# Kernel tuning notes

Measured on AMD Instinct MI355X. Metric: run time of the kernel, lower is better.

Reference implementation:

```python
import jax, jax.numpy as jnp
from jax import lax
import numpy as np

NUM_CLASS = 80
N_PROP = 256
C_FEAT, H_FEAT, W_FEAT = 1024, 50, 80
IMG_H, IMG_W = 800, 1280
POOL = 14
SPATIAL_SCALE = 0.0625
SCORE_THR = 0.5
NMS_THR = 0.7
K_PRE = 1000   # pre-NMS candidate cap (jit-static stand-in for boolean filter)
K_OUT = 200    # keep[:200] in source
BW = (10.0, 10.0, 5.0, 5.0)
SCALE_CLAMP = float(np.log(1000.0 / 16.0))


def setup_inputs() -> dict:
    key = jax.random.key(0)
    ks = jax.random.split(key, 9)
    features = jax.random.normal(ks[0], (1, C_FEAT, H_FEAT, W_FEAT), jnp.float32)
    x1 = jax.random.uniform(ks[1], (N_PROP,), minval=0.0, maxval=IMG_W - 64.0)
    y1 = jax.random.uniform(ks[2], (N_PROP,), minval=0.0, maxval=IMG_H - 64.0)
    w = jax.random.uniform(ks[3], (N_PROP,), minval=32.0, maxval=320.0)
    h = jax.random.uniform(ks[4], (N_PROP,), minval=32.0, maxval=320.0)
    proposals = jnp.stack([x1, y1, jnp.minimum(x1 + w, float(IMG_W)),
                           jnp.minimum(y1 + h, float(IMG_H))], axis=1)
    d_in = C_FEAT * POOL * POOL
    w_fc = jax.random.normal(ks[5], (d_in, 1024), jnp.float32) / np.sqrt(d_in)
    b_fc = jnp.zeros((1024,), jnp.float32)
    # scale class head up so softmax produces confident (>0.5) detections
    w_cls = jax.random.normal(ks[6], (1024, NUM_CLASS + 1), jnp.float32) * (8.0 / np.sqrt(1024))
    b_cls = jnp.zeros((NUM_CLASS + 1,), jnp.float32)
    w_box = jax.random.normal(ks[7], (1024, NUM_CLASS * 4), jnp.float32) / np.sqrt(1024)
    b_box = jnp.zeros((NUM_CLASS * 4,), jnp.float32)
    return {"features": features, "proposals": proposals, "w_fc": w_fc, "b_fc": b_fc,
            "w_cls": w_cls, "b_cls": b_cls, "w_box": w_box, "b_box": b_box}


def roi_align(features, rois):
    """torchvision RoIAlign (aligned=False), output 14x14, one sample per bin.
    features: [1,C,H,W], rois: [N,4] xyxy. Returns [N,C,14,14]."""
    f = features[0]                               # [C,H,W]
    H, W = f.shape[1], f.shape[2]
    x1 = rois[:, 0] * SPATIAL_SCALE
    y1 = rois[:, 1] * SPATIAL_SCALE
    x2 = rois[:, 2] * SPATIAL_SCALE
    y2 = rois[:, 3] * SPATIAL_SCALE
    rw = jnp.maximum(x2 - x1, 1.0)
    rh = jnp.maximum(y2 - y1, 1.0)
    bw = rw / POOL
    bh = rh / POOL
    grid = jnp.arange(POOL, dtype=jnp.float32) + 0.5
    xs = x1[:, None] + grid[None, :] * bw[:, None]      # [N,P] bin-center x
    ys = y1[:, None] + grid[None, :] * bh[:, None]      # [N,P] bin-center y
    Y = jnp.broadcast_to(ys[:, :, None], (rois.shape[0], POOL, POOL))
    X = jnp.broadcast_to(xs[:, None, :], (rois.shape[0], POOL, POOL))
    valid = (Y >= -1.0) & (Y <= H) & (X >= -1.0) & (X <= W)
    y = jnp.clip(Y, 0.0, H - 1.0)
    x = jnp.clip(X, 0.0, W - 1.0)
    y0 = jnp.floor(y).astype(jnp.int32)
    x0 = jnp.floor(x).astype(jnp.int32)
    y1i = jnp.minimum(y0 + 1, H - 1)
    x1i = jnp.minimum(x0 + 1, W - 1)
    ly = y - y0; lx = x - x0; hy = 1.0 - ly; hx = 1.0 - lx
    g = lambda yi, xi: f[:, yi, xi]               # -> [C,N,P,P]
    val = ((hy * hx) * g(y0, x0) + (hy * lx) * g(y0, x1i)
           + (ly * hx) * g(y1i, x0) + (ly * lx) * g(y1i, x1i))
    val = val * valid.astype(val.dtype)
    return jnp.transpose(val, (1, 0, 2, 3))       # [N,C,P,P]


def apply_deltas(boxes, deltas):
    """boxes,deltas: [..., 4]; detectron-style delta apply with weights BW."""
    w = boxes[..., 2] - boxes[..., 0]
    h = boxes[..., 3] - boxes[..., 1]
    cx = boxes[..., 0] + 0.5 * w
    cy = boxes[..., 1] + 0.5 * h
    dx = deltas[..., 0] / BW[0]
    dy = deltas[..., 1] / BW[1]
    dw = jnp.minimum(deltas[..., 2] / BW[2], SCALE_CLAMP)
    dh = jnp.minimum(deltas[..., 3] / BW[3], SCALE_CLAMP)
    pcx = dx * w + cx
    pcy = dy * h + cy
    pw = jnp.exp(dw) * w
    ph = jnp.exp(dh) * h
    return jnp.stack([pcx - 0.5 * pw, pcy - 0.5 * ph,
                      pcx + 0.5 * pw, pcy + 0.5 * ph], axis=-1)


def _iou_matrix(b):
    area = jnp.maximum(b[:, 2] - b[:, 0], 0.0) * jnp.maximum(b[:, 3] - b[:, 1], 0.0)
    lt = jnp.maximum(b[:, None, :2], b[None, :, :2])
    rb = jnp.minimum(b[:, None, 2:], b[None, :, 2:])
    wh = jnp.clip(rb - lt, 0.0)
    inter = wh[..., 0] * wh[..., 1]
    return inter / jnp.maximum(area[:, None] + area[None, :] - inter, 1e-9)


def forward(features, proposals, w_fc, b_fc, w_cls, b_cls, w_box, b_box):
    feat = roi_align(features, proposals)                 # [N,1024,14,14]
    x = feat.reshape(feat.shape[0], -1) @ w_fc + b_fc     # [N,1024]
    logits = x @ w_cls + b_cls                            # [N,81]
    deltas = x @ w_box + b_box                            # [N,320]
    scores = jax.nn.softmax(logits, axis=-1)[:, 1:]       # [N,80] drop bg

    # per-class box-delta apply (proposal expanded over classes)
    boxes = apply_deltas(jnp.broadcast_to(proposals[:, None, :], (N_PROP, NUM_CLASS, 4)),
                         deltas.reshape(N_PROP, NUM_CLASS, 4))
    boxes = jnp.stack([jnp.clip(boxes[..., 0], 0.0, float(IMG_W)),
                       jnp.clip(boxes[..., 1], 0.0, float(IMG_H)),
                       jnp.clip(boxes[..., 2], 0.0, float(IMG_W)),
                       jnp.clip(boxes[..., 3], 0.0, float(IMG_H))], axis=-1)

    # flatten (proposal, class) candidates; mask = score > 0.5 (boolean filter in source)
    s_flat = scores.reshape(-1)
    b_flat = boxes.reshape(-1, 4)
    c_flat = jnp.broadcast_to(jnp.arange(NUM_CLASS)[None, :], (N_PROP, NUM_CLASS)).reshape(-1)
    masked = jnp.where(s_flat > SCORE_THR, s_flat, -1.0)
    top_s, top_i = lax.top_k(masked, K_PRE)              # score-sorted candidates
    cand_b = b_flat[top_i]
    cand_c = c_flat[top_i]
    cand_valid = top_s > SCORE_THR

    # batched NMS: offset boxes by class so classes never interact
    off = cand_c.astype(jnp.float32) * float(IMG_W + 1)
    iou = _iou_matrix(cand_b + off[:, None])
    idxs = jnp.arange(K_PRE)

    def body(keep, xs):
        i, row = xs
        kept_i = keep[i]
        suppress = kept_i & (row > NMS_THR) & (idxs > i)
        return keep & ~suppress, kept_i

    _, kept = lax.scan(body, cand_valid, (idxs, iou))

    # compact kept candidates (already score-ordered) into top-200 slots
    rank = jnp.cumsum(kept.astype(jnp.int32)) - 1
    slot = jnp.where(kept, rank, K_OUT)  # out-of-range -> dropped
    out_boxes = jnp.zeros((K_OUT, 4), cand_b.dtype).at[slot].set(cand_b, mode='drop')
    out_scores = jnp.zeros((K_OUT,), top_s.dtype).at[slot].set(top_s, mode='drop')
    out_classes = jnp.full((K_OUT,), -1, jnp.int32).at[slot].set(cand_c.astype(jnp.int32), mode='drop')
    return out_boxes, out_scores, out_classes


def reference(features, proposals, w_fc, b_fc, w_cls, b_cls, w_box, b_box):
    return forward(features, proposals, w_fc, b_fc, w_cls, b_cls, w_box, b_box)
```

## Files before the change

kernel.cpp:

```cpp
#include <hip/hip_runtime.h>
#include <math.h>

#define N_PROP 256
#define NUM_CLASS 80
#define H_FEAT 50
#define W_FEAT 80
#define K_DIM 200704
#define D_HID 1024
#define SPATIAL_SCALE 0.0625f
#define SCALE_CLAMP 4.135166556742356f
#define IMG_W_F 1280.0f
#define IMG_H_F 800.0f

typedef unsigned short ushort_t;
typedef __attribute__((ext_vector_type(8))) short short8v;
typedef __attribute__((ext_vector_type(16))) float f32x16;
typedef __attribute__((ext_vector_type(4))) float f32x4v;
typedef __attribute__((ext_vector_type(4))) unsigned short ushort4v;
typedef __attribute__((ext_vector_type(2))) unsigned short ushort2v;

__device__ __forceinline__ unsigned short f2bf(float f) {
  unsigned int u = __builtin_bit_cast(unsigned int, f);
  u += 0x7FFFu + ((u >> 16) & 1u);
  return (unsigned short)(u >> 16);
}
__device__ __forceinline__ float bf2f(unsigned short h) {
  unsigned int u = ((unsigned int)h) << 16;
  return __builtin_bit_cast(float, u);
}

__global__ void roi_kernel(const float* __restrict__ F, const float* __restrict__ props,
                           ushort_t* __restrict__ Ahi, ushort_t* __restrict__ Alo) {
  const int tid = threadIdx.x;
  const int m = blockIdx.y;
  const int cg = blockIdx.x;
  __shared__ float w00[196], w01[196], w10[196], w11[196];
  __shared__ int o00[196], o01[196], o10[196], o11[196];
  const float x1s = props[m*4+0]*SPATIAL_SCALE;
  const float y1s = props[m*4+1]*SPATIAL_SCALE;
  const float x2s = props[m*4+2]*SPATIAL_SCALE;
  const float y2s = props[m*4+3]*SPATIAL_SCALE;
  const float bwf = fmaxf(x2s-x1s, 1.0f) / 14.0f;
  const float bhf = fmaxf(y2s-y1s, 1.0f) / 14.0f;
  if (tid < 196) {
    int ph = tid / 14, pw = tid - ph*14;
    float X = x1s + (pw + 0.5f)*bwf;
    float Y = y1s + (ph + 0.5f)*bhf;
    bool valid = (Y >= -1.0f) && (Y <= (float)H_FEAT) && (X >= -1.0f) && (X <= (float)W_FEAT);
    float x = fminf(fmaxf(X, 0.0f), (float)(W_FEAT-1));
    float y = fminf(fmaxf(Y, 0.0f), (float)(H_FEAT-1));
    float xf = floorf(x), yf = floorf(y);
    int ix0 = (int)xf, iy0 = (int)yf;
    int ix1 = min(ix0+1, W_FEAT-1), iy1 = min(iy0+1, H_FEAT-1);
    float lx = x-xf, ly = y-yf, hx = 1.0f-lx, hy = 1.0f-ly;
    float v = valid ? 1.0f : 0.0f;
    w00[tid] = hy*hx*v; w01[tid] = hy*lx*v; w10[tid] = ly*hx*v; w11[tid] = ly*lx*v;
    o00[tid] = iy0*W_FEAT+ix0; o01[tid] = iy0*W_FEAT+ix1;
    o10[tid] = iy1*W_FEAT+ix0; o11[tid] = iy1*W_FEAT+ix1;
  }
  __syncthreads();
  const int base_c = cg*128;
  const size_t rowbase = (size_t)m*K_DIM + (size_t)base_c*196;
  for (int it = 0; it < 49; ++it) {
    int i2 = it*512 + tid*2;
    int c = i2 / 196;
    int b = i2 - c*196;
    const float* f = F + (size_t)(base_c + c)*4000;
    float v0 = w00[b]*f[o00[b]] + w01[b]*f[o01[b]] + w10[b]*f[o10[b]] + w11[b]*f[o11[b]];
    float v1 = w00[b+1]*f[o00[b+1]] + w01[b+1]*f[o01[b+1]] + w10[b+1]*f[o10[b+1]] + w11[b+1]*f[o11[b+1]];
    unsigned short h0 = f2bf(v0), h1 = f2bf(v1);
    ushort2v hv; hv[0] = h0; hv[1] = h1;
    ushort2v lv; lv[0] = f2bf(v0 - bf2f(h0)); lv[1] = f2bf(v1 - bf2f(h1));
    *(ushort2v*)&Ahi[rowbase + i2] = hv;
    *(ushort2v*)&Alo[rowbase + i2] = lv;
  }
}

__global__ __launch_bounds__(512, 2) void mfma_gemm(
    const ushort_t* __restrict__ Ahi, const ushort_t* __restrict__ Alo,
    const float* __restrict__ B, float* __restrict__ P, int steps_per, int nwg) {
  __shared__ ushort_t lds[40960];
  const int tid = threadIdx.x;
  const int wv = tid >> 6, lane = tid & 63, l31 = lane & 31, lhi = lane >> 5;
  const int wm = wv >> 2, wn = wv & 3;
  int id = blockIdx.x;
  int nid = ((nwg & 7) == 0) ? ((id & 7) * (nwg >> 3) + (id >> 3)) : id;
  const int bn = (nid & 3) * 256;
  const int z  = nid >> 2;
  const int step0 = z * steps_per;
  int steps = steps_per;
  if (step0 + steps > 6272) steps = 6272 - step0;

  f32x16 acc[4][2];
  #pragma unroll
  for (int a = 0; a < 4; ++a)
    #pragma unroll
    for (int b = 0; b < 2; ++b)
      #pragma unroll
      for (int e = 0; e < 16; ++e) acc[a][b][e] = 0.0f;

  if (steps > 0) {
    const int H = steps * 2;
    const ushort_t* asrc[2];
    #pragma unroll
    for (int i = 0; i < 2; ++i) {
      int s = i*512 + tid;
      int plane = s >> 9, kb = (s >> 8) & 1, row = s & 255;
      const ushort_t* basep = plane ? Alo : Ahi;
      asrc[i] = basep + (size_t)row * K_DIM + step0*32 + kb*8;
    }
    const int p = tid >> 6, c4 = tid & 63;
    const bool bstage = (tid < 256);
    const float* bsrc = B + (size_t)(step0*32 + 4*p) * D_HID + bn + c4*4;
    const unsigned bkbh = (unsigned)(p >> 1) * 2048u, bsub = (unsigned)((p & 1) * 4);

    #define STAGE_A(aoff) do { \
      _Pragma("unroll") \
      for (int i = 0; i < 2; ++i) { \
        __builtin_amdgcn_global_load_lds(asrc[i], &lds[(aoff) + (unsigned)(i*512 + tid)*8u], 16, 0, 0); \
        asrc[i] += 16; } \
    } while (0)

    #define LOAD_B() do { \
      if (bstage) { \
        b0 = __builtin_nontemporal_load((const f32x4v*)(bsrc)); \
        b1 = __builtin_nontemporal_load((const f32x4v*)(bsrc + D_HID)); \
        b2 = __builtin_nontemporal_load((const f32x4v*)(bsrc + 2*D_HID)); \
        b3 = __builtin_nontemporal_load((const f32x4v*)(bsrc + 3*D_HID)); \
      } \
      bsrc += 16 * D_HID; \
    } while (0)

    #define WRITE_B(boff) do { \
      if (bstage) { \
        _Pragma("unroll") \
        for (int cc = 0; cc < 4; ++cc) { \
          float g0 = b0[cc], g1 = b1[cc], g2 = b2[cc], g3 = b3[cc]; \
          ushort4v hv, lv; \
          hv[0]=f2bf(g0); lv[0]=f2bf(g0-bf2f(hv[0])); \
          hv[1]=f2bf(g1); lv[1]=f2bf(g1-bf2f(hv[1])); \
          hv[2]=f2bf(g2); lv[2]=f2bf(g2-bf2f(hv[2])); \
          hv[3]=f2bf(g3); lv[3]=f2bf(g3-bf2f(hv[3])); \
          int col = c4*4 + cc, scol = col ^ ((col>>3)&7); \
          unsigned idx = (boff) + bkbh + (unsigned)scol*8u + bsub; \
          *(ushort4v*)&lds[idx] = hv; \
          *(ushort4v*)&lds[idx + 4096] = lv; \
        } \
      } \
    } while (0)

    #define COMPUTE(aoff, boff) do { \
      short8v ah[4], al[4], bh[2], bl[2]; \
      _Pragma("unroll") \
      for (int ms = 0; ms < 4; ++ms) { \
        unsigned ai = (aoff) + (unsigned)(lhi*2048 + (wm*128 + ms*32 + l31)*8); \
        ah[ms] = *(const short8v*)&lds[ai]; \
        al[ms] = *(const short8v*)&lds[ai + 4096]; \
      } \
      _Pragma("unroll") \
      for (int ns = 0; ns < 2; ++ns) { \
        int col = wn*64 + ns*32 + l31, scol = col ^ ((col>>3)&7); \
        unsigned bi = (boff) + (unsigned)(lhi*2048 + scol*8); \
        bh[ns] = *(const short8v*)&lds[bi]; \
        bl[ns] = *(const short8v*)&lds[bi + 4096]; \
      } \
      __builtin_amdgcn_s_setprio(1); \
      _Pragma("unroll") \
      for (int ms = 0; ms < 4; ++ms) \
        _Pragma("unroll") \
        for (int ns = 0; ns < 2; ++ns) { \
          acc[ms][ns] = __builtin_amdgcn_mfma_f32_32x32x16_bf16(ah[ms], bh[ns], acc[ms][ns], 0, 0, 0); \
          acc[ms][ns] = __builtin_amdgcn_mfma_f32_32x32x16_bf16(ah[ms], bl[ns], acc[ms][ns], 0, 0, 0); \
          acc[ms][ns] = __builtin_amdgcn_mfma_f32_32x32x16_bf16(al[ms], bh[ns], acc[ms][ns], 0, 0, 0); \
        } \
      __builtin_amdgcn_s_setprio(0); \
    } while (0)

    f32x4v b0, b1, b2, b3;
    LOAD_B();
    STAGE_A(0u);
    STAGE_A(8192u);
    asm volatile("s_waitcnt vmcnt(4)" ::: "memory");
    __builtin_amdgcn_sched_barrier(0);
    WRITE_B(24576u);
    asm volatile("s_waitcnt vmcnt(2)" ::: "memory");
    asm volatile("s_waitcnt lgkmcnt(0)" ::: "memory");
    __builtin_amdgcn_s_barrier();
    __builtin_amdgcn_sched_barrier(0);

    unsigned aC = 0u, aN = 8192u, aNN = 16384u;
    unsigned bC = 24576u, bN = 32768u;
    for (int h = 0; h < H; ++h) {
      const int rem = H - 1 - h;
      if (rem > 0) LOAD_B();
      if (rem > 1) STAGE_A(aNN);
      COMPUTE(aC, bC);
      if (rem > 1)       asm volatile("s_waitcnt vmcnt(2)" ::: "memory");
      else if (rem == 1) asm volatile("s_waitcnt vmcnt(0)" ::: "memory");
      __builtin_amdgcn_sched_barrier(0);
      if (rem > 0) WRITE_B(bN);
      asm volatile("s_waitcnt lgkmcnt(0)" ::: "memory");
      __builtin_amdgcn_s_barrier();
      __builtin_amdgcn_sched_barrier(0);
      unsigned t = aC; aC = aN; aN = aNN; aNN = t;
      t = bC; bC = bN; bN = t;
    }
    #undef STAGE_A
    #undef LOAD_B
    #undef WRITE_B
    #undef COMPUTE
  }
  float* Pp = P + (size_t)z * (N_PROP * D_HID);
  #pragma unroll
  for (int ms = 0; ms < 4; ++ms)
    #pragma unroll
    for (int ns = 0; ns < 2; ++ns)
      #pragma unroll
      for (int r = 0; r < 16; ++r) {
        int row = wm*128 + ms*32 + (r & 3) + 8*(r >> 2) + 4*lhi;
        int col = bn + wn*64 + ns*32 + l31;
        __builtin_nontemporal_store(acc[ms][ns][r], &Pp[(size_t)row * D_HID + col]);
      }
}

__global__ void reduce_kernel(const float* __restrict__ P, float* __restrict__ X, int ksplit) {
  int i = blockIdx.x*256 + threadIdx.x;
  f32x4v s = {0.0f, 0.0f, 0.0f, 0.0f};
  const f32x4v* P4 = (const f32x4v*)P;
  for (int r = 0; r < ksplit; ++r) s += P4[(size_t)r*65536 + i];
  ((f32x4v*)X)[i] = s;
}

__global__ void heads_kernel(const float* __restrict__ X, const float* __restrict__ bfc,
                             const float* __restrict__ wcls, const float* __restrict__ bcls,
                             const float* __restrict__ wbox, const float* __restrict__ bbox,
                             float* __restrict__ scores, float* __restrict__ deltas,
                             float* __restrict__ keym) {
  const int tid = threadIdx.x, m = blockIdx.x;
  __shared__ float xs[1024];
  __shared__ float lg[81];
  __shared__ float red[2];
  #pragma unroll
  for (int r = 0; r < 4; ++r) {
    int k = r*256 + tid;
    xs[k] = X[m*1024 + k] + bfc[k];
  }
  __syncthreads();
  for (int j = tid; j < 401; j += 256) {
    if (j < 81) {
      const float* w = wcls + j;
      float accv = bcls[j];
      #pragma unroll 8
      for (int k = 0; k < 1024; ++k) accv = fmaf(xs[k], w[(size_t)k*81], accv);
      lg[j] = accv;
    } else {
      int jb = j - 81;
      const float* w = wbox + jb;
      float accv = bbox[jb];
      #pragma unroll 8
      for (int k = 0; k < 1024; ++k) accv = fmaf(xs[k], w[(size_t)k*320], accv);
      deltas[m*320 + jb] = accv;
    }
  }
  __syncthreads();
  if (tid == 0) {
    float mx = lg[0]; int amax = 0;
    for (int j = 1; j < 81; ++j) if (lg[j] > mx) { mx = lg[j]; amax = j; }
    float sm = 0.0f;
    for (int j = 0; j < 81; ++j) sm += expf(lg[j]-mx);
    float m2 = -1e30f;
    for (int j = 0; j < 81; ++j) if (j != amax) m2 = fmaxf(m2, lg[j]);
    float s2 = 0.0f;
    for (int j = 0; j < 81; ++j) if (j != amax) s2 += expf(lg[j]-m2);
    keym[m] = (m2 - mx) + logf(s2);
    red[0] = mx; red[1] = sm;
  }
  __syncthreads();
  if (tid < 80) scores[m*80 + tid] = expf(lg[tid+1]-red[0]) / red[1];
}

__global__ void detect_kernel(const float* __restrict__ scores, const float* __restrict__ deltas,
                              const float* __restrict__ props, const float* __restrict__ keym,
                              float* __restrict__ out) {
  const int tid = threadIdx.x;
  __shared__ int s_cnt;
  __shared__ float g_key[256];
  __shared__ float g_score[256];
  __shared__ int   g_idx[256];
  __shared__ float c_score[256];
  __shared__ int   c_idx[256];
  __shared__ float bxs[256][4];
  __shared__ int   bcls[256];
  __shared__ unsigned long long supp[256][4];
  if (tid == 0) s_cnt = 0;
  g_key[tid] = 1e30f; g_score[tid] = -1.0f; g_idx[tid] = 0x7FFFFFFF;
  c_score[tid] = -1.0f; c_idx[tid] = 0x7FFFFFFF;
  bxs[tid][0] = bxs[tid][1] = bxs[tid][2] = bxs[tid][3] = 0.0f;
  bcls[tid] = 0;
  __syncthreads();
  for (int t = 0; t < 80; ++t) {
    int i = t*256 + tid;
    float s = scores[i];
    if (s > 0.5f) {
      int p = atomicAdd(&s_cnt, 1);
      if (p < 256) { g_score[p] = s; g_idx[p] = i; g_key[p] = keym[i/80]; }
    }
  }
  __syncthreads();
  const int C = min(s_cnt, 256);
  if (tid < C) {
    float kt = g_key[tid]; int si = g_idx[tid]; float st = g_score[tid];
    int rank = 0;
    for (int u = 0; u < C; ++u) {
      float ku = g_key[u]; int iu = g_idx[u];
      if ((ku < kt) || (ku == kt && iu < si)) ++rank;
    }
    c_score[rank] = st; c_idx[rank] = si;
  }
  __syncthreads();
  if (tid < C) {
    int fi = c_idx[tid];
    int m = fi / 80, j = fi - m*80;
    float px1 = props[m*4+0], py1 = props[m*4+1], px2 = props[m*4+2], py2 = props[m*4+3];
    float w = px2-px1, h = py2-py1;
    float cx = px1 + 0.5f*w, cy = py1 + 0.5f*h;
    const float* d = deltas + m*320 + j*4;
    float dx = d[0]/10.0f, dy = d[1]/10.0f;
    float dw = fminf(d[2]/5.0f, SCALE_CLAMP), dh = fminf(d[3]/5.0f, SCALE_CLAMP);
    float pcx = dx*w + cx, pcy = dy*h + cy;
    float pw = expf(dw)*w, ph = expf(dh)*h;
    bxs[tid][0] = fminf(fmaxf(pcx - 0.5f*pw, 0.0f), IMG_W_F);
    bxs[tid][1] = fminf(fmaxf(pcy - 0.5f*ph, 0.0f), IMG_H_F);
    bxs[tid][2] = fminf(fmaxf(pcx + 0.5f*pw, 0.0f), IMG_W_F);
    bxs[tid][3] = fminf(fmaxf(pcy + 0.5f*ph, 0.0f), IMG_H_F);
    bcls[tid] = j;
  }
  __syncthreads();
  unsigned long long row[4] = {0,0,0,0};
  if (tid < C) {
    float ax1=bxs[tid][0], ay1=bxs[tid][1], ax2=bxs[tid][2], ay2=bxs[tid][3];
    float aarea = fmaxf(ax2-ax1,0.f)*fmaxf(ay2-ay1,0.f);
    int acl = bcls[tid];
    for (int j2 = tid+1; j2 < C; ++j2) {
      if (bcls[j2] != acl) continue;
      float b1=bxs[j2][0], b2=bxs[j2][1], b3=bxs[j2][2], b4=bxs[j2][3];
      float barea = fmaxf(b3-b1,0.f)*fmaxf(b4-b2,0.f);
      float iw = fmaxf(fminf(ax2,b3) - fmaxf(ax1,b1), 0.f);
      float ih = fmaxf(fminf(ay2,b4) - fmaxf(ay1,b2), 0.f);
      float inter = iw*ih;
      float iou = inter / fmaxf(aarea + barea - inter, 1e-9f);
      if (iou > 0.7f) row[j2>>6] |= (1ull << (j2 & 63));
    }
  }
  supp[tid][0]=row[0]; supp[tid][1]=row[1]; supp[tid][2]=row[2]; supp[tid][3]=row[3];
  __syncthreads();
  for (int i = tid; i < 1200; i += 256) out[i] = (i >= 1000) ? -1.0f : 0.0f;
  __syncthreads();
  if (tid == 0) {
    unsigned long long rem[4] = {0,0,0,0};
    int oc = 0;
    for (int i = 0; i < C; ++i) {
      if ((rem[i>>6] >> (i & 63)) & 1ull) continue;
      if (oc < 200) {
        out[oc*4+0]=bxs[i][0]; out[oc*4+1]=bxs[i][1]; out[oc*4+2]=bxs[i][2]; out[oc*4+3]=bxs[i][3];
        out[800+oc]  = c_score[i];
        out[1000+oc] = (float)bcls[i];
      }
      ++oc;
      rem[0]|=supp[i][0]; rem[1]|=supp[i][1]; rem[2]|=supp[i][2]; rem[3]|=supp[i][3];
    }
  }
}

extern "C" void kernel_launch(void* const* d_in, const int* in_sizes, int n_in,
                              void* d_out, int out_size, void* d_ws, size_t ws_size,
                              hipStream_t stream) {
  const float* F     = (const float*)d_in[0];
  const float* props = (const float*)d_in[1];
  const float* wfc   = (const float*)d_in[2];
  const float* bfc   = (const float*)d_in[3];
  const float* wcls  = (const float*)d_in[4];
  const float* bcls  = (const float*)d_in[5];
  const float* wbox  = (const float*)d_in[6];
  const float* bbox  = (const float*)d_in[7];
  float* out = (float*)d_out;
  char* wsb  = (char*)d_ws;

  const size_t abytes = (size_t)N_PROP * K_DIM * 2;
  ushort_t* Ahi = (ushort_t*)wsb;
  ushort_t* Alo = (ushort_t*)(wsb + abytes);
  float* X  = (float*)(wsb + 2*abytes);
  float* SC = X + 262144;
  float* DL = SC + 20480;
  float* KM = DL + 81920;
  float* P  = KM + 256;
  const size_t fixed = 2*abytes + (size_t)(262144 + 20480 + 81920 + 256) * 4;
  if (ws_size < fixed + 2u*1048576u) {
    (void)hipMemsetAsync(d_out, 0x7F, (size_t)out_size*sizeof(float), stream);
    return;
  }
  int ksplit = (int)((ws_size - fixed) / ((size_t)N_PROP * D_HID * 4));
  if (ksplit > 64) ksplit = 64;
  if (ksplit >= 8) ksplit &= ~7;
  const int steps_per = (6272 + ksplit - 1) / ksplit;
  const int nwg = 4 * ksplit;

  roi_kernel   <<<dim3(8, N_PROP),    256, 0, stream>>>(F, props, Ahi, Alo);
  mfma_gemm    <<<nwg,                512, 0, stream>>>(Ahi, Alo, wfc, P, steps_per, nwg);
  reduce_kernel<<<256,                256, 0, stream>>>(P, X, ksplit);
  heads_kernel <<<N_PROP,             256, 0, stream>>>(X, bfc, wcls, bcls, wbox, bbox, SC, DL, KM);
  detect_kernel<<<1,                  256, 0, stream>>>(SC, DL, props, KM, out);
}
```

Measured before the change: 798.4 us.

## Deepen GEMM software pipeline to prefetch A and B two stages ahead

Adds a fourth LDS buffer for the A tile and a second register set for the B tile, and unrolls the main loop by two so global loads are issued two iterations ahead of compute instead of one. This is meant to hide more global-memory latency behind the MFMA work. In exchange LDS use grows from 80KB to 96KB per block and more vector registers are held live, which can lower occupancy or cause spills. The waitcnt bookkeeping also becomes more intricate.

```diff
diff --git a/kernel.cpp b/kernel.cpp
--- a/kernel.cpp
+++ b/kernel.cpp
@@ -79,7 +79,7 @@
 __global__ __launch_bounds__(512, 2) void mfma_gemm(
     const ushort_t* __restrict__ Ahi, const ushort_t* __restrict__ Alo,
     const float* __restrict__ B, float* __restrict__ P, int steps_per, int nwg) {
-  __shared__ ushort_t lds[40960];
+  __shared__ ushort_t lds[49152];
   const int tid = threadIdx.x;
   const int wv = tid >> 6, lane = tid & 63, l31 = lane & 31, lhi = lane >> 5;
   const int wm = wv >> 2, wn = wv & 3;
@@ -121,21 +121,21 @@
         asrc[i] += 16; } \
     } while (0)
 
-    #define LOAD_B() do { \
+    #define LOAD_B(s0,s1,s2,s3) do { \
       if (bstage) { \
-        b0 = __builtin_nontemporal_load((const f32x4v*)(bsrc)); \
-        b1 = __builtin_nontemporal_load((const f32x4v*)(bsrc + D_HID)); \
-        b2 = __builtin_nontemporal_load((const f32x4v*)(bsrc + 2*D_HID)); \
-        b3 = __builtin_nontemporal_load((const f32x4v*)(bsrc + 3*D_HID)); \
+        s0 = __builtin_nontemporal_load((const f32x4v*)(bsrc)); \
+        s1 = __builtin_nontemporal_load((const f32x4v*)(bsrc + D_HID)); \
+        s2 = __builtin_nontemporal_load((const f32x4v*)(bsrc + 2*D_HID)); \
+        s3 = __builtin_nontemporal_load((const f32x4v*)(bsrc + 3*D_HID)); \
       } \
       bsrc += 16 * D_HID; \
     } while (0)
 
-    #define WRITE_B(boff) do { \
+    #define WRITE_B(boff,s0,s1,s2,s3) do { \
       if (bstage) { \
         _Pragma("unroll") \
         for (int cc = 0; cc < 4; ++cc) { \
-          float g0 = b0[cc], g1 = b1[cc], g2 = b2[cc], g3 = b3[cc]; \
+          float g0 = s0[cc], g1 = s1[cc], g2 = s2[cc], g3 = s3[cc]; \
           ushort4v hv, lv; \
           hv[0]=f2bf(g0); lv[0]=f2bf(g0-bf2f(hv[0])); \
           hv[1]=f2bf(g1); lv[1]=f2bf(g1-bf2f(hv[1])); \
@@ -176,34 +176,55 @@
       __builtin_amdgcn_s_setprio(0); \
     } while (0)
 
-    f32x4v b0, b1, b2, b3;
-    LOAD_B();
+    f32x4v x0, x1, x2, x3;
+    f32x4v y0, y1, y2, y3;
+    LOAD_B(x0,x1,x2,x3);
     STAGE_A(0u);
     STAGE_A(8192u);
     asm volatile("s_waitcnt vmcnt(4)" ::: "memory");
     __builtin_amdgcn_sched_barrier(0);
-    WRITE_B(24576u);
-    asm volatile("s_waitcnt vmcnt(2)" ::: "memory");
+    WRITE_B(32768u, x0,x1,x2,x3);
+    LOAD_B(y0,y1,y2,y3);
+    if (H > 2) {
+      STAGE_A(16384u);
+      asm volatile("s_waitcnt vmcnt(8)" ::: "memory");
+    } else {
+      asm volatile("s_waitcnt vmcnt(6)" ::: "memory");
+    }
     asm volatile("s_waitcnt lgkmcnt(0)" ::: "memory");
     __builtin_amdgcn_s_barrier();
     __builtin_amdgcn_sched_barrier(0);
 
-    unsigned aC = 0u, aN = 8192u, aNN = 16384u;
-    unsigned bC = 24576u, bN = 32768u;
-    for (int h = 0; h < H; ++h) {
-      const int rem = H - 1 - h;
-      if (rem > 0) LOAD_B();
-      if (rem > 1) STAGE_A(aNN);
-      COMPUTE(aC, bC);
-      if (rem > 1)       asm volatile("s_waitcnt vmcnt(2)" ::: "memory");
-      else if (rem == 1) asm volatile("s_waitcnt vmcnt(0)" ::: "memory");
-      __builtin_amdgcn_sched_barrier(0);
-      if (rem > 0) WRITE_B(bN);
-      asm volatile("s_waitcnt lgkmcnt(0)" ::: "memory");
-      __builtin_amdgcn_s_barrier();
-      __builtin_amdgcn_sched_barrier(0);
-      unsigned t = aC; aC = aN; aN = aNN; aNN = t;
-      t = bC; bC = bN; bN = t;
+    unsigned aC = 0u, aN = 8192u, aNN = 16384u, aNNN = 24576u;
+    for (int h = 0; h < H; h += 2) {
+      {
+        const int rem = H - 1 - h;
+        if (rem >= 2) LOAD_B(x0,x1,x2,x3);
+        if (rem >= 3) STAGE_A(aNNN);
+        COMPUTE(aC, 32768u);
+        if (rem >= 2) asm volatile("s_waitcnt vmcnt(6)" ::: "memory");
+        else          asm volatile("s_waitcnt vmcnt(0)" ::: "memory");
+        __builtin_amdgcn_sched_barrier(0);
+        if (rem >= 1) WRITE_B(40960u, y0,y1,y2,y3);
+        asm volatile("s_waitcnt lgkmcnt(0)" ::: "memory");
+        __builtin_amdgcn_s_barrier();
+        __builtin_amdgcn_sched_barrier(0);
+        unsigned t = aC; aC = aN; aN = aNN; aNN = aNNN; aNNN = t;
+      }
+      if (h + 1 < H) {
+        const int rem = H - 2 - h;
+        if (rem >= 2) LOAD_B(y0,y1,y2,y3);
+        if (rem >= 3) STAGE_A(aNNN);
+        COMPUTE(aC, 40960u);
+        if (rem >= 2) asm volatile("s_waitcnt vmcnt(6)" ::: "memory");
+        else          asm volatile("s_waitcnt vmcnt(0)" ::: "memory");
+        __builtin_amdgcn_sched_barrier(0);
+        if (rem >= 1) WRITE_B(32768u, x0,x1,x2,x3);
+        asm volatile("s_waitcnt lgkmcnt(0)" ::: "memory");
+        __builtin_amdgcn_s_barrier();
+        __builtin_amdgcn_sched_barrier(0);
+        unsigned t = aC; aC = aN; aN = aNN; aNN = aNNN; aNNN = t;
+      }
     }
     #undef STAGE_A
     #undef LOAD_B
```

New measurement: 794.8 us. No clear change (-0.5%).
